# Kernel optimization log

Hardware: AMD Instinct MI355X
Metric: run time of the kernel (lower is better)

## Reference

```python
import jax, jax.numpy as jnp
import numpy as np
from jax import lax

GRID_W, GRID_H = 4, 4
N_NODES = GRID_W * GRID_H  # 16
N_NEIGH = 8
N_CLS = 10
BN_EPS = 1e-5


def _neighbors(i, w, h, mode=8):
    # exact port of Brain.neighbors (ordering matters for the concat)
    size = w * h
    out = []
    if i - w >= 0:
        out.append(i - w)
    if i % w != 0:
        out.append(i - 1)
    if (i + 1) % w != 0:
        out.append(i + 1)
    if i + w < size:
        out.append(i + w)
    if mode == 8:
        if i - w - 1 >= 0 and i % w != 0:
            out.append(i - w - 1)
        if i - w + 1 >= 0 and (i + 1) % w != 0:
            out.append(i - w + 1)
        if i + w - 1 < size and i % w != 0:
            out.append(i + w - 1)
        if i + w + 1 < size and (i + 1) % w != 0:
            out.append(i + w + 1)
    return out


def _neighbor_table():
    idx = np.full((N_NODES, N_NEIGH), 0, dtype=np.int32)
    mask = np.zeros((N_NODES, N_NEIGH), dtype=np.float32)
    for i in range(N_NODES):
        n = _neighbors(i, GRID_W, GRID_H, 8)
        idx[i, :len(n)] = np.array(n, dtype=np.int32)
        mask[i, :len(n)] = 1.0
    return jnp.asarray(idx), jnp.asarray(mask)


def _conv(x, w, b):
    y = lax.conv_general_dilated(x, w, (1, 1), 'SAME',
                                 dimension_numbers=('NCHW', 'OIHW', 'NCHW'))
    return y + b[None, :, None, None]


def _bn_train(x, g, b):
    # BatchNorm2d in training mode (module default): batch statistics
    mean = jnp.mean(x, axis=(0, 2, 3), keepdims=True)
    var = jnp.var(x, axis=(0, 2, 3), keepdims=True)
    xn = (x - mean) * lax.rsqrt(var + BN_EPS)
    return xn * g[None, :, None, None] + b[None, :, None, None]


def _maxpool(x):
    # MaxPool2d(kernel=3, stride=2, padding=1)
    return lax.reduce_window(x, -jnp.inf, lax.max,
                             (1, 1, 3, 3), (1, 1, 2, 2),
                             ((0, 0), (0, 0), (1, 1), (1, 1)))


def setup_inputs() -> dict:
    key = jax.random.key(0)
    ks = jax.random.split(key, 24)
    B = 128
    f32 = jnp.float32

    def rn(k, shape, scale):
        return jax.random.normal(k, shape, dtype=f32) * scale

    inp = {
        'x': rn(ks[0], (B, 3, 64, 64), 1.0),
        'cw1': rn(ks[1], (64, 3, 3, 3), 0.1), 'cb1': jnp.zeros((64,), f32),
        'bn1_g': jnp.ones((64,), f32), 'bn1_b': jnp.zeros((64,), f32),
        'cw2': rn(ks[2], (128, 64, 3, 3), 0.05), 'cb2': jnp.zeros((128,), f32),
        'bn2_g': jnp.ones((128,), f32), 'bn2_b': jnp.zeros((128,), f32),
        'cw3': rn(ks[3], (256, 128, 3, 3), 0.03), 'cb3': jnp.zeros((256,), f32),
        'cw4': rn(ks[4], (256, 256, 3, 3), 0.02), 'cb4': jnp.zeros((256,), f32),
        'cw5': rn(ks[5], (512, 256, 3, 3), 0.02), 'cb5': jnp.zeros((512,), f32),
        'cw6': rn(ks[6], (512, 512, 3, 3), 0.015), 'cb6': jnp.zeros((512,), f32),
        'cw7': rn(ks[7], (512, 512, 3, 3), 0.015), 'cb7': jnp.zeros((512,), f32),
        'W1': rn(ks[8], (N_NODES, 592, 600), 0.04), 'b1': jnp.zeros((N_NODES, 600), f32),
        'W2': rn(ks[9], (N_NODES, 600, N_CLS), 0.04), 'b2': jnp.zeros((N_NODES, N_CLS), f32),
    }
    return inp


def _backbone(x, cw1, cb1, bn1_g, bn1_b, cw2, cb2, bn2_g, bn2_b,
              cw3, cb3, cw4, cb4, cw5, cb5, cw6, cb6, cw7, cb7):
    h = _maxpool(jax.nn.relu(_bn_train(_conv(x, cw1, cb1), bn1_g, bn1_b)))
    h = _maxpool(jax.nn.relu(_bn_train(_conv(h, cw2, cb2), bn2_g, bn2_b)))
    h = jax.nn.relu(_conv(h, cw3, cb3))
    h = _maxpool(jax.nn.relu(_conv(h, cw4, cb4)))
    h = jax.nn.relu(_conv(h, cw5, cb5))
    h = _maxpool(jax.nn.relu(_conv(h, cw6, cb6)))
    h = jax.nn.relu(_conv(h, cw7, cb7))
    return h  # [B, 512, 4, 4]


def _colons(X, W1, b1, W2, b2):
    # X: [16, B, 592] -> softmax probs [16, B, 10]; per-node MLP
    h = jnp.tanh(jnp.einsum('nbi,nio->nbo', X, W1) + b1[:, None, :])
    logits = jnp.einsum('nbh,nho->nbo', h, W2) + b2[:, None, :]
    return jax.nn.softmax(logits, axis=-1)


def reference(x, cw1, cb1, bn1_g, bn1_b, cw2, cb2, bn2_g, bn2_b,
              cw3, cb3, cw4, cb4, cw5, cb5, cw6, cb6, cw7, cb7,
              W1, b1, W2, b2):
    B = x.shape[0]
    conv = _backbone(x, cw1, cb1, bn1_g, bn1_b, cw2, cb2, bn2_g, bn2_b,
                     cw3, cb3, cw4, cb4, cw5, cb5, cw6, cb6, cw7, cb7)
    conv = conv.reshape(B, 512, N_NODES)           # torch.flatten(conv, 2)
    feats = jnp.transpose(conv, (2, 0, 1))         # [16, B, 512]

    # first pass: neighbor slots are all-zero p1..p8
    zeros80 = jnp.zeros((N_NODES, B, N_NEIGH * N_CLS), dtype=x.dtype)
    preds1 = _colons(jnp.concatenate([zeros80, feats], axis=-1), W1, b1, W2, b2)

    # second pass: gather neighbor predictions (zero-padded to 8 slots)
    idx, mask = _neighbor_table()                  # [16,8] int, [16,8] float
    gathered = preds1[idx]                         # [16, 8, B, 10]
    gathered = gathered * mask[:, :, None, None]
    neigh = jnp.transpose(gathered, (0, 2, 1, 3)).reshape(N_NODES, B, N_NEIGH * N_CLS)
    preds2 = _colons(jnp.concatenate([neigh, feats], axis=-1), W1, b1, W2, b2)  # [16, B, 10]

    sum_preds = jnp.mean(preds2, axis=0)           # [B, 10]
    squared_sum_preds = sum_preds * sum_preds
    return squared_sum_preds, preds2
```

## Files before the change

### kernel.cpp

```cpp
#include <hip/hip_runtime.h>
#include <math.h>


#define BN_EPS 1e-5f

typedef _Float16 f16x8 __attribute__((ext_vector_type(8)));
typedef _Float16 f16x4 __attribute__((ext_vector_type(4)));
typedef float    f32x4v __attribute__((ext_vector_type(4)));

constexpr int ilog2c(int x) { return x <= 1 ? 0 : 1 + ilog2c(x >> 1); }

__device__ __forceinline__ void lds_barrier() {
    asm volatile("s_waitcnt lgkmcnt(0)\n\ts_barrier" ::: "memory");
}

__global__ __launch_bounds__(256)
void wprep_kernel(const float* __restrict__ cw1, const float* __restrict__ cw2,
                  const float* __restrict__ cw3, const float* __restrict__ cw4,
                  const float* __restrict__ cw5, const float* __restrict__ cw6,
                  const float* __restrict__ cw7, _Float16* __restrict__ wreg)
{
    const int layer = blockIdx.y;
    const int t = blockIdx.x * 256 + threadIdx.x;
    if (layer == 0) {
        if (t < 64) {
#pragma unroll
            for (int k = 0; k < 32; ++k)
                wreg[t * 32 + k] = (k < 27) ? (_Float16)cw1[t * 27 + k] : (_Float16)0.f;
        }
        return;
    }
    const float* src = nullptr;
    _Float16* dst = nullptr;
    int n = 0;
    switch (layer) {
        case 1: src = cw2; dst = wreg + 2048;    n = 8192;   break;
        case 2: src = cw3; dst = wreg + 75776;   n = 32768;  break;
        case 3: src = cw4; dst = wreg + 370688;  n = 65536;  break;
        case 4: src = cw5; dst = wreg + 960512;  n = 131072; break;
        case 5: src = cw6; dst = wreg + 2140160; n = 262144; break;
        case 6: src = cw7; dst = wreg + 4499456; n = 262144; break;
    }
    if (t >= n) return;
#pragma unroll
    for (int ph = 0; ph < 9; ++ph)
        dst[ph * n + t] = (_Float16)src[t * 9 + ph];
}

__global__ __launch_bounds__(256)
void w1t_kernel(const float* __restrict__ W1, _Float16* __restrict__ Tf,
                _Float16* __restrict__ Tn)
{
    __shared__ float T[64][65];
    const int n  = blockIdx.z;
    const int o0 = blockIdx.y * 64;
    const int k0 = blockIdx.x * 64;
    const int tid = threadIdx.x;
    const int c  = tid & 63;
    const int r4 = tid >> 6;
    const float* Wn = W1 + (size_t)n * 592 * 600;
#pragma unroll
    for (int rep = 0; rep < 16; ++rep) {
        const int kr = rep * 4 + r4;
        const int k = k0 + kr, o = o0 + c;
        float v = 0.f;
        if (k < 592 && o < 600) v = Wn[k * 600 + o];
        T[kr][c] = v;
    }
    __syncthreads();
#pragma unroll
    for (int rep = 0; rep < 16; ++rep) {
        const int orr = rep * 4 + r4;
        const int o = o0 + orr;
        const int k = k0 + c;
        const float v = T[c][orr];
        if (k >= 80 && k < 592)
            Tf[((size_t)(n * 640 + o)) * 512 + (k - 80)] = (_Float16)v;
        if (k < 96)
            Tn[((size_t)(n * 640 + o)) * 96 + k] = (k < 80) ? (_Float16)v : (_Float16)0.f;
    }
}

__global__ void b1pad_kernel(const float* __restrict__ b1, float* __restrict__ b1p)
{
    const int t = blockIdx.x * 256 + threadIdx.x;
    if (t >= 16 * 640) return;
    const int n = t / 640, o = t - n * 640;
    b1p[t] = (o < 600) ? b1[n * 600 + o] : 0.f;
}

__global__ __launch_bounds__(256)
void conv1_mfma_kernel(const float* __restrict__ in, const _Float16* __restrict__ w32,
                       _Float16* __restrict__ out, int B)
{
    __shared__ __align__(16) _Float16 As[64 * 32];
    __shared__ __align__(16) _Float16 Bs[128 * 32];

    const int tid  = threadIdx.x;
    const int pix0 = blockIdx.x * 128;
    const int bn   = tid & 127;
    const int bh   = tid >> 7;
    const int gp   = pix0 + bn;
    const int pb   = gp >> 12;
    const int sp   = gp & 4095;
    const int py   = sp >> 6;
    const int px   = sp & 63;
    const float* inb = in + (size_t)pb * 3 * 4096;

    _Float16 vals[16];
    if (bh == 0) {
#pragma unroll
        for (int u = 0; u < 16; ++u) {
            const int k = u;
            const int ci = k / 9, r = k - ci * 9, ky = r / 3, kx = r - ky * 3;
            const int iy = py + ky - 1, ix = px + kx - 1;
            float v = 0.f;
            if ((unsigned)iy < 64u && (unsigned)ix < 64u)
                v = inb[ci * 4096 + iy * 64 + ix];
            vals[u] = (_Float16)v;
        }
    } else {
#pragma unroll
        for (int u = 0; u < 16; ++u) {
            const int k = 16 + u;
            float v = 0.f;
            if (k < 27) {
                const int ci = k / 9, r = k - ci * 9, ky = r / 3, kx = r - ky * 3;
                const int iy = py + ky - 1, ix = px + kx - 1;
                if ((unsigned)iy < 64u && (unsigned)ix < 64u)
                    v = inb[ci * 4096 + iy * 64 + ix];
            }
            vals[u] = (_Float16)v;
        }
    }
    f16x8 b0, b1;
#pragma unroll
    for (int j = 0; j < 8; ++j) { b0[j] = vals[j]; b1[j] = vals[8 + j]; }
    *(f16x8*)&Bs[bn * 32 + (((2 * bh    ) ^ (bn & 3)) << 3)] = b0;
    *(f16x8*)&Bs[bn * 32 + (((2 * bh + 1) ^ (bn & 3)) << 3)] = b1;

    if (tid < 128) {
        const int arow = tid >> 1, ah = tid & 1;
        const f16x8 a0 = *(const f16x8*)(w32 + arow * 32 + ah * 16);
        const f16x8 a1 = *(const f16x8*)(w32 + arow * 32 + ah * 16 + 8);
        *(f16x8*)&As[arow * 32 + (((2 * ah    ) ^ (arow & 3)) << 3)] = a0;
        *(f16x8*)&As[arow * 32 + (((2 * ah + 1) ^ (arow & 3)) << 3)] = a1;
    }
    __syncthreads();

    const int lane = tid & 63, wv = tid >> 6;
    const int q = lane >> 4, lm = lane & 15;
    const int swz = (q ^ (lm & 3)) << 3;

    f16x8 af[4], bf[2];
#pragma unroll
    for (int ti = 0; ti < 4; ++ti)
        af[ti] = *(const f16x8*)&As[(ti * 16 + lm) * 32 + swz];
#pragma unroll
    for (int tj = 0; tj < 2; ++tj)
        bf[tj] = *(const f16x8*)&Bs[(wv * 32 + tj * 16 + lm) * 32 + swz];

    f32x4v acc[4][2];
#pragma unroll
    for (int ti = 0; ti < 4; ++ti)
#pragma unroll
        for (int tj = 0; tj < 2; ++tj)
            acc[ti][tj] = __builtin_amdgcn_mfma_f32_16x16x32_f16(
                af[ti], bf[tj], (f32x4v)0.f, 0, 0, 0);

#pragma unroll
    for (int tj = 0; tj < 2; ++tj) {
        const int gpix = pix0 + wv * 32 + tj * 16 + lm;
#pragma unroll
        for (int ti = 0; ti < 4; ++ti) {
            const int cob = ti * 16 + q * 4;
            f16x4 h4;
#pragma unroll
            for (int r = 0; r < 4; ++r) h4[r] = (_Float16)acc[ti][tj][r];
            *(f16x4*)&out[(size_t)gpix * 64 + cob] = h4;
        }
    }
}

template <int CI, int CO, int H, int W, int KSPLIT, int EPI>
__global__ __launch_bounds__(256)
void conv_p2_kernel(const _Float16* __restrict__ in, const _Float16* __restrict__ w9,
                    const float* __restrict__ bias, _Float16* __restrict__ out,
                    float* __restrict__ part, const _Float16* __restrict__ zbuf, int B)
{
    constexpr int HW   = H * W;
    constexpr int lgHW = ilog2c(HW);
    constexpr int lgW  = ilog2c(W);

    __shared__ __align__(16) _Float16 As[3][128 * 32];
    __shared__ __align__(16) _Float16 Bs[3][128 * 32];

    const int tid  = threadIdx.x;
    const int pix0 = blockIdx.x * 128;
    const int co0  = blockIdx.y * 128;

    const int lane = tid & 63, wv = tid >> 6;
    const int wm = (wv & 1) * 64, wn = (wv >> 1) * 64;
    const int q = lane >> 4, lm = lane & 15;
    const int swz = (q ^ (lm & 3)) << 3;

    const int arow = tid >> 1, ah = tid & 1;
    const int aw0 = ((2 * ah    ) ^ (arow & 3)) << 3;
    const int aw1 = ((2 * ah + 1) ^ (arow & 3)) << 3;
    const _Float16* abase = w9 + ((size_t)(co0 + arow)) * CI + ah * 16;

    const int bn = tid & 127, bh = tid >> 7;
    const int gp = pix0 + bn;
    const int pb = gp >> lgHW;
    const int spx = gp & (HW - 1);
    const int py = spx >> lgW, px = spx & (W - 1);
    const int bw0 = ((2 * bh    ) ^ (bn & 3)) << 3;
    const int bw1 = ((2 * bh + 1) ^ (bn & 3)) << 3;

    constexpr int CS_TOT = CI / 32;
    constexpr int CS_PER = CS_TOT / KSPLIT;
    constexpr int NIT    = 9 * CS_PER;
    const int cs0 = (KSPLIT > 1) ? blockIdx.z * CS_PER : 0;

    const _Float16* bstage;
    auto setB = [&](int phx) {
        const int dy = phx / 3 - 1;
        const int dx = phx - (phx / 3) * 3 - 1;
        const int y2 = py + dy, x2 = px + dx;
        const bool valid = ((unsigned)y2 < (unsigned)H) && ((unsigned)x2 < (unsigned)W);
        const int sp2 = (y2 << lgW) | x2;
        bstage = valid ? (in + ((size_t)((pb << lgHW) | sp2)) * CI + bh * 16)
                       : (zbuf + bh * 16);
    };

    f32x4v acc[4][4];
#pragma unroll
    for (int i = 0; i < 4; ++i)
#pragma unroll
        for (int j = 0; j < 4; ++j) acc[i][j] = (f32x4v)0.f;

    f16x8 aq[2][2], bq[2][2];
    int lph = 0, lcs = 0;
    setB(0);
    auto loadT = [&](int s) {
        const _Float16* ap = abase + (size_t)lph * CO * CI + (size_t)(cs0 + lcs) * 32;
        aq[s][0] = *(const f16x8*)ap;
        aq[s][1] = *(const f16x8*)(ap + 8);
        const _Float16* bp2 = bstage + (size_t)(cs0 + lcs) * 32;
        bq[s][0] = *(const f16x8*)bp2;
        bq[s][1] = *(const f16x8*)(bp2 + 8);
        if (++lcs == CS_PER) { lcs = 0; ++lph; if (lph < 9) setB(lph); }
    };
    loadT(0);
    loadT(1);
    *(f16x8*)&As[0][arow * 32 + aw0] = aq[0][0];
    *(f16x8*)&As[0][arow * 32 + aw1] = aq[0][1];
    *(f16x8*)&Bs[0][bn * 32 + bw0]   = bq[0][0];
    *(f16x8*)&Bs[0][bn * 32 + bw1]   = bq[0][1];

#pragma unroll 6
    for (int it = 0; it < NIT; ++it) {
        if (it + 2 < NIT) loadT(it & 1);
        if (it + 1 < NIT) {
            const int s1 = (it + 1) & 1;
            const int wb = (it + 1) % 3;
            *(f16x8*)&As[wb][arow * 32 + aw0] = aq[s1][0];
            *(f16x8*)&As[wb][arow * 32 + aw1] = aq[s1][1];
            *(f16x8*)&Bs[wb][bn * 32 + bw0]   = bq[s1][0];
            *(f16x8*)&Bs[wb][bn * 32 + bw1]   = bq[s1][1];
        }
        lds_barrier();
        const int rb = it % 3;
        f16x8 afr[4], bfr[4];
#pragma unroll
        for (int ti = 0; ti < 4; ++ti)
            afr[ti] = *(const f16x8*)&As[rb][(wm + ti * 16 + lm) * 32 + swz];
#pragma unroll
        for (int tj = 0; tj < 4; ++tj)
            bfr[tj] = *(const f16x8*)&Bs[rb][(wn + tj * 16 + lm) * 32 + swz];
#pragma unroll
        for (int ti = 0; ti < 4; ++ti)
#pragma unroll
            for (int tj = 0; tj < 4; ++tj)
                acc[ti][tj] = __builtin_amdgcn_mfma_f32_16x16x32_f16(
                    afr[ti], bfr[tj], acc[ti][tj], 0, 0, 0);
    }

    if (EPI == 2) {
        float* pout = part + (size_t)blockIdx.z * ((size_t)B * HW * CO);
#pragma unroll
        for (int tj = 0; tj < 4; ++tj) {
            const int gpix = pix0 + wn + tj * 16 + lm;
#pragma unroll
            for (int ti = 0; ti < 4; ++ti) {
                const int cob = co0 + wm + ti * 16 + q * 4;
                *(float4*)&pout[(size_t)gpix * CO + cob] =
                    make_float4(acc[ti][tj][0], acc[ti][tj][1],
                                acc[ti][tj][2], acc[ti][tj][3]);
            }
        }
    } else {
#pragma unroll
        for (int tj = 0; tj < 4; ++tj) {
            const int gpix = pix0 + wn + tj * 16 + lm;
#pragma unroll
            for (int ti = 0; ti < 4; ++ti) {
                const int cob = co0 + wm + ti * 16 + q * 4;
                f16x4 h4;
                if (EPI == 1) {
                    const float4 bb4 = *(const float4*)&bias[cob];
                    h4[0] = (_Float16)fmaxf(acc[ti][tj][0] + bb4.x, 0.f);
                    h4[1] = (_Float16)fmaxf(acc[ti][tj][1] + bb4.y, 0.f);
                    h4[2] = (_Float16)fmaxf(acc[ti][tj][2] + bb4.z, 0.f);
                    h4[3] = (_Float16)fmaxf(acc[ti][tj][3] + bb4.w, 0.f);
                } else {
#pragma unroll
                    for (int r = 0; r < 4; ++r) h4[r] = (_Float16)acc[ti][tj][r];
                }
                *(f16x4*)&out[(size_t)gpix * CO + cob] = h4;
            }
        }
    }
}

template <int C>
__global__ __launch_bounds__(256)
void bn_stats_nhwc_kernel(const _Float16* __restrict__ in, float* __restrict__ sums,
                          int Ptot)
{
    constexpr int C8 = C / 8;
    constexpr int PS = 256 / C8;
    const int chunk = Ptot / gridDim.x;
    const int c8   = threadIdx.x & (C8 - 1);
    const int poff = threadIdx.x >> ilog2c(C8);
    float s[8], s2[8];
#pragma unroll
    for (int j = 0; j < 8; ++j) { s[j] = 0.f; s2[j] = 0.f; }
    const int p0 = blockIdx.x * chunk;
    for (int p = p0 + poff; p < p0 + chunk; p += PS) {
        const f16x8 v = *(const f16x8*)(in + (size_t)p * C + c8 * 8);
#pragma unroll
        for (int j = 0; j < 8; ++j) {
            const float f = (float)v[j];
            s[j] += f; s2[j] += f * f;
        }
    }
    __shared__ float ls[2 * C];
    for (int i = threadIdx.x; i < 2 * C; i += 256) ls[i] = 0.f;
    __syncthreads();
#pragma unroll
    for (int j = 0; j < 8; ++j) {
        atomicAdd(&ls[c8 * 8 + j], s[j]);
        atomicAdd(&ls[C + c8 * 8 + j], s2[j]);
    }
    __syncthreads();
    for (int i = threadIdx.x; i < 2 * C; i += 256) atomicAdd(&sums[i], ls[i]);
}

template <int C>
__global__ void bn_finalize_kernel(const float* __restrict__ sums,
                                   const float* __restrict__ g,
                                   const float* __restrict__ beta,
                                   float* __restrict__ ss, int Ntot)
{
    const int c = blockIdx.x * 64 + threadIdx.x;
    if (c >= C) return;
    const float inv   = 1.f / (float)Ntot;
    const float mean  = sums[c] * inv;
    const float var   = sums[C + c] * inv - mean * mean;
    const float scale = g[c] * rsqrtf(var + BN_EPS);
    ss[c]     = scale;
    ss[C + c] = beta[c] - mean * scale;
}

template <int C, int Hin, int Win, bool DO_BN>
__global__ __launch_bounds__(256)
void pool_nhwc_kernel(const _Float16* __restrict__ in, const float* __restrict__ ss,
                      _Float16* __restrict__ out, int B)
{
    constexpr int Ho = Hin / 2, Wo = Win / 2, C8 = C / 8;
    constexpr int lgC8 = ilog2c(C8), lgWo = ilog2c(Wo), lgHo = ilog2c(Ho);
    const int t = blockIdx.x * 256 + threadIdx.x;
    const int total = B * Ho * Wo * C8;
    if (t >= total) return;
    const int c8 = t & (C8 - 1);
    const int r1 = t >> lgC8;
    const int ox = r1 & (Wo - 1);
    const int r2 = r1 >> lgWo;
    const int oy = r2 & (Ho - 1);
    const int b  = r2 >> lgHo;

    float sc[8], sh[8];
    if (DO_BN) {
#pragma unroll
        for (int j = 0; j < 8; ++j) {
            sc[j] = ss[c8 * 8 + j];
            sh[j] = ss[C + c8 * 8 + j];
        }
    }
    float m[8];
#pragma unroll
    for (int j = 0; j < 8; ++j) m[j] = -1e30f;

    const int y0 = max(0, 2 * oy - 1), y1 = min(Hin - 1, 2 * oy + 1);
    const int x0 = max(0, 2 * ox - 1), x1 = min(Win - 1, 2 * ox + 1);
    const _Float16* ib = in + ((size_t)b * Hin * Win) * C + c8 * 8;
    for (int iy = y0; iy <= y1; ++iy)
        for (int ix = x0; ix <= x1; ++ix) {
            const f16x8 v = *(const f16x8*)(ib + (size_t)(iy * Win + ix) * C);
#pragma unroll
            for (int j = 0; j < 8; ++j) {
                float f = (float)v[j];
                if (DO_BN) f = f * sc[j] + sh[j];
                m[j] = fmaxf(m[j], f);
            }
        }
    f16x8 o;
#pragma unroll
    for (int j = 0; j < 8; ++j) {
        float f = m[j];
        if (DO_BN) f = fmaxf(f, 0.f);
        o[j] = (_Float16)f;
    }
    *(f16x8*)&out[((size_t)((b << (lgHo + lgWo)) | (oy << lgWo) | ox)) * C + c8 * 8] = o;
}

template <int CO, int Z>
__global__ __launch_bounds__(256)
void sum_bias_relu_nhwc_kernel(const float* __restrict__ part, const float* __restrict__ bias,
                               _Float16* __restrict__ out, int Npix)
{
    const int t = blockIdx.x * 256 + threadIdx.x;
    const int N8 = Npix * CO / 8;
    if (t >= N8) return;
    const size_t i8 = (size_t)t * 8;
    const int c = (int)(i8 & (CO - 1));
    const size_t S = (size_t)Npix * CO;
    float4 x0 = *(const float4*)(part + i8);
    float4 x1 = *(const float4*)(part + i8 + 4);
#pragma unroll
    for (int z = 1; z < Z; ++z) {
        const float4 p0 = *(const float4*)(part + z * S + i8);
        const float4 p1 = *(const float4*)(part + z * S + i8 + 4);
        x0.x += p0.x; x0.y += p0.y; x0.z += p0.z; x0.w += p0.w;
        x1.x += p1.x; x1.y += p1.y; x1.z += p1.z; x1.w += p1.w;
    }
    const float4 b0 = *(const float4*)(bias + c);
    const float4 b1 = *(const float4*)(bias + c + 4);
    f16x8 o;
    o[0] = (_Float16)fmaxf(x0.x + b0.x, 0.f);
    o[1] = (_Float16)fmaxf(x0.y + b0.y, 0.f);
    o[2] = (_Float16)fmaxf(x0.z + b0.z, 0.f);
    o[3] = (_Float16)fmaxf(x0.w + b0.w, 0.f);
    o[4] = (_Float16)fmaxf(x1.x + b1.x, 0.f);
    o[5] = (_Float16)fmaxf(x1.y + b1.y, 0.f);
    o[6] = (_Float16)fmaxf(x1.z + b1.z, 0.f);
    o[7] = (_Float16)fmaxf(x1.w + b1.w, 0.f);
    *(f16x8*)&out[i8] = o;
}

template <int Z>
__global__ __launch_bounds__(256)
void build_xf_kernel(const float* __restrict__ part, const float* __restrict__ bias,
                     _Float16* __restrict__ Xf, int B)
{
    const int t = blockIdx.x * 256 + threadIdx.x;
    if (t >= B * 16 * 128) return;
    const int pix = t >> 7;
    const int c   = (t & 127) * 4;
    const size_t S = (size_t)B * 16 * 512;
    float4 a = *(const float4*)(part + (size_t)pix * 512 + c);
#pragma unroll
    for (int z = 1; z < Z; ++z) {
        const float4 p = *(const float4*)(part + z * S + (size_t)pix * 512 + c);
        a.x += p.x; a.y += p.y; a.z += p.z; a.w += p.w;
    }
    const float4 bb = *(const float4*)(bias + c);
    f16x4 o4;
    o4[0] = (_Float16)fmaxf(a.x + bb.x, 0.f);
    o4[1] = (_Float16)fmaxf(a.y + bb.y, 0.f);
    o4[2] = (_Float16)fmaxf(a.z + bb.z, 0.f);
    o4[3] = (_Float16)fmaxf(a.w + bb.w, 0.f);
    const int b_ = pix >> 4, sp = pix & 15;
    *(f16x4*)&Xf[((size_t)(sp * B + b_)) * 512 + c] = o4;
}

template <int K, bool PASS2>
__global__ __launch_bounds__(256)
void fc1_mfma_kernel(const _Float16* __restrict__ Xf, const _Float16* __restrict__ W1T,
                     const float* __restrict__ b1p, float* __restrict__ pre,
                     float* __restrict__ h, int B)
{
    __shared__ __align__(16) _Float16 As[2][128 * 32];
    __shared__ __align__(16) _Float16 Bs[2][128 * 32];

    const int tid = threadIdx.x;
    const int o0  = blockIdx.x * 128;
    const int n   = blockIdx.y;

    const int lane = tid & 63, wv = tid >> 6;
    const int wm = (wv & 1) * 64, wn = (wv >> 1) * 64;
    const int q = lane >> 4, lm = lane & 15;
    const int swz = (q ^ (lm & 3)) << 3;

    const int arow = tid >> 1, ah = tid & 1;
    const int aw0 = ((2 * ah    ) ^ (arow & 3)) << 3;
    const int aw1 = ((2 * ah + 1) ^ (arow & 3)) << 3;

    const _Float16* asrc = W1T + ((size_t)(n * 640 + o0 + arow)) * K + ah * 16;
    const _Float16* bsrc = Xf  + ((size_t)(n * 128 + arow)) * K + ah * 16;

    f32x4v acc[4][4];
#pragma unroll
    for (int i = 0; i < 4; ++i)
#pragma unroll
        for (int j = 0; j < 4; ++j) acc[i][j] = (f32x4v)0.f;

    constexpr int S = K / 32;
    {
        const f16x8 a0 = *(const f16x8*)(asrc);
        const f16x8 a1 = *(const f16x8*)(asrc + 8);
        const f16x8 b0 = *(const f16x8*)(bsrc);
        const f16x8 b1 = *(const f16x8*)(bsrc + 8);
        *(f16x8*)&As[0][arow * 32 + aw0] = a0;
        *(f16x8*)&As[0][arow * 32 + aw1] = a1;
        *(f16x8*)&Bs[0][arow * 32 + aw0] = b0;
        *(f16x8*)&Bs[0][arow * 32 + aw1] = b1;
    }
    int buf = 0;
    for (int s = 0; s < S; ++s) {
        f16x8 aN0, aN1, bN0, bN1;
        if (s + 1 < S) {
            aN0 = *(const f16x8*)(asrc + (s + 1) * 32);
            aN1 = *(const f16x8*)(asrc + (s + 1) * 32 + 8);
            bN0 = *(const f16x8*)(bsrc + (s + 1) * 32);
            bN1 = *(const f16x8*)(bsrc + (s + 1) * 32 + 8);
        }
        lds_barrier();
        f16x8 afr[4], bfr[4];
#pragma unroll
        for (int ti = 0; ti < 4; ++ti)
            afr[ti] = *(const f16x8*)&As[buf][(wm + ti * 16 + lm) * 32 + swz];
#pragma unroll
        for (int tj = 0; tj < 4; ++tj)
            bfr[tj] = *(const f16x8*)&Bs[buf][(wn + tj * 16 + lm) * 32 + swz];
#pragma unroll
        for (int ti = 0; ti < 4; ++ti)
#pragma unroll
            for (int tj = 0; tj < 4; ++tj)
                acc[ti][tj] = __builtin_amdgcn_mfma_f32_16x16x32_f16(
                    afr[ti], bfr[tj], acc[ti][tj], 0, 0, 0);
        if (s + 1 < S) {
            *(f16x8*)&As[buf ^ 1][arow * 32 + aw0] = aN0;
            *(f16x8*)&As[buf ^ 1][arow * 32 + aw1] = aN1;
            *(f16x8*)&Bs[buf ^ 1][arow * 32 + aw0] = bN0;
            *(f16x8*)&Bs[buf ^ 1][arow * 32 + aw1] = bN1;
            buf ^= 1;
        }
    }

#pragma unroll
    for (int tj = 0; tj < 4; ++tj) {
        const int m = wn + tj * 16 + lm;
#pragma unroll
        for (int ti = 0; ti < 4; ++ti) {
            const int o = o0 + wm + ti * 16 + q * 4;
            const size_t oi = ((size_t)(n * 128 + m)) * 640 + o;
            float4 base;
            if (PASS2) base = *(const float4*)&pre[oi];
            else       base = *(const float4*)&b1p[n * 640 + o];
            float4 v = make_float4(acc[ti][tj][0] + base.x, acc[ti][tj][1] + base.y,
                                   acc[ti][tj][2] + base.z, acc[ti][tj][3] + base.w);
            if (!PASS2) *(float4*)&pre[oi] = v;
            *(float4*)&h[oi] = make_float4(tanhf(v.x), tanhf(v.y), tanhf(v.z), tanhf(v.w));
        }
    }
}

__global__ __launch_bounds__(128)
void colon_fc2_kernel(const float* __restrict__ h, const float* __restrict__ W2,
                      const float* __restrict__ b2, float* __restrict__ preds, int B)
{
    const int n = blockIdx.x;
    __shared__ float W2s[6000];
    __shared__ float b2s[10];
    for (int i = threadIdx.x; i < 6000; i += 128) W2s[i] = W2[n * 6000 + i];
    if (threadIdx.x < 10) b2s[threadIdx.x] = b2[n * 10 + threadIdx.x];
    __syncthreads();

    for (int b = threadIdx.x; b < B; b += 128) {
        float l[10];
#pragma unroll
        for (int c = 0; c < 10; ++c) l[c] = b2s[c];
        const float* hp = h + ((size_t)(n * B + b)) * 640;
        for (int k = 0; k < 600; k += 4) {
            const float4 hv = *reinterpret_cast<const float4*>(&hp[k]);
            const float hh[4] = {hv.x, hv.y, hv.z, hv.w};
#pragma unroll
            for (int u = 0; u < 4; ++u)
#pragma unroll
                for (int c = 0; c < 10; ++c)
                    l[c] += hh[u] * W2s[(k + u) * 10 + c];
        }
        float mx = l[0];
#pragma unroll
        for (int c = 1; c < 10; ++c) mx = fmaxf(mx, l[c]);
        float s = 0.f;
#pragma unroll
        for (int c = 0; c < 10; ++c) { l[c] = expf(l[c] - mx); s += l[c]; }
        const float inv = 1.f / s;
        float* pp = preds + ((size_t)(n * B + b)) * 10;
#pragma unroll
        for (int c = 0; c < 10; ++c) pp[c] = l[c] * inv;
    }
}

__global__ __launch_bounds__(256)
void fill_neigh_kernel(const float* __restrict__ preds1, _Float16* __restrict__ Xn, int B)
{
    const int t = blockIdx.x * 256 + threadIdx.x;
    if (t >= 16 * B * 96) return;
    const int col = t % 96;
    const int b   = (t / 96) % B;
    const int n   = t / (96 * B);

    float v = 0.f;
    if (col < 80) {
        const int j = col / 10, c = col - j * 10;
        int lst[8];
        int cnt = 0;
        const int w = 4, sz = 16, i = n;
        if (i - w >= 0)                                lst[cnt++] = i - w;
        if (i % w != 0)                                lst[cnt++] = i - 1;
        if ((i + 1) % w != 0)                          lst[cnt++] = i + 1;
        if (i + w < sz)                                lst[cnt++] = i + w;
        if (i - w - 1 >= 0 && i % w != 0)              lst[cnt++] = i - w - 1;
        if (i - w + 1 >= 0 && (i + 1) % w != 0)        lst[cnt++] = i - w + 1;
        if (i + w - 1 < sz && i % w != 0)              lst[cnt++] = i + w - 1;
        if (i + w + 1 < sz && (i + 1) % w != 0)        lst[cnt++] = i + w + 1;
        if (j < cnt) v = preds1[((size_t)(lst[j] * B + b)) * 10 + c];
    }
    Xn[t] = (_Float16)v;
}

__global__ __launch_bounds__(256)
void final_out_kernel(const float* __restrict__ preds2, float* __restrict__ out0, int B)
{
    const int t = blockIdx.x * 256 + threadIdx.x;
    if (t >= B * 10) return;
    const int b = t / 10, c = t % 10;
    float s = 0.f;
#pragma unroll
    for (int n = 0; n < 16; ++n)
        s += preds2[((size_t)(n * B + b)) * 10 + c];
    const float m = s * (1.f / 16.f);
    out0[t] = m * m;
}

extern "C" void kernel_launch(void* const* d_in, const int* in_sizes, int n_in,
                              void* d_out, int out_size, void* d_ws, size_t ws_size,
                              hipStream_t stream)
{
    const float* x    = (const float*)d_in[0];
    const float* cw1  = (const float*)d_in[1];
    const float* bn1g = (const float*)d_in[3];
    const float* bn1b = (const float*)d_in[4];
    const float* cw2  = (const float*)d_in[5];
    const float* bn2g = (const float*)d_in[7];
    const float* bn2b = (const float*)d_in[8];
    const float* cw3  = (const float*)d_in[9];
    const float* cb3  = (const float*)d_in[10];
    const float* cw4  = (const float*)d_in[11];
    const float* cb4  = (const float*)d_in[12];
    const float* cw5  = (const float*)d_in[13];
    const float* cb5  = (const float*)d_in[14];
    const float* cw6  = (const float*)d_in[15];
    const float* cb6  = (const float*)d_in[16];
    const float* cw7  = (const float*)d_in[17];
    const float* cb7  = (const float*)d_in[18];
    const float* W1   = (const float*)d_in[19];
    const float* b1   = (const float*)d_in[20];
    const float* W2   = (const float*)d_in[21];
    const float* b2   = (const float*)d_in[22];

    const int B = in_sizes[0] / (3 * 64 * 64);

    float* ws = (float*)d_ws;
    float*     P    = ws;
    _Float16*  A    = (_Float16*)(ws + 8388608);
    _Float16*  Bb   = (_Float16*)(ws + 25165824);
    _Float16*  wreg = (_Float16*)(ws + 33554432);
    _Float16*  W1Tf = (_Float16*)(ws + 36984832);
    _Float16*  W1Tn = (_Float16*)(ws + 39606272);
    _Float16*  Xf16 = (_Float16*)(ws + 40097792);
    _Float16*  Xn16 = (_Float16*)(ws + 40622080);
    float*     b1p  = ws + 40720384;
    float*     preb = ws + 40730624;
    float*     hb   = ws + 42041344;
    float*     small= ws + 43352064;
    float* sums1  = small;
    float* sums2  = small + 256;
    float* ss1    = small + 1024;
    float* ss2    = small + 1536;
    float* preds1 = small + 2048;
    _Float16* zbuf = (_Float16*)(small + 32768);

    float* out0   = (float*)d_out;
    float* preds2 = (float*)d_out + (size_t)B * 10;

    hipMemsetAsync(small, 0, 512 * sizeof(float), stream);
    hipMemsetAsync(zbuf, 0, 4096, stream);

    wprep_kernel<<<dim3(1024, 7), 256, 0, stream>>>(cw1, cw2, cw3, cw4, cw5, cw6, cw7, wreg);
    w1t_kernel<<<dim3(10, 10, 16), 256, 0, stream>>>(W1, W1Tf, W1Tn);
    b1pad_kernel<<<(16 * 640 + 255) / 256, 256, 0, stream>>>(b1, b1p);

    _Float16* w1f  = wreg;
    _Float16* w9c2 = wreg + 2048;
    _Float16* w9c3 = wreg + 75776;
    _Float16* w9c4 = wreg + 370688;
    _Float16* w9c5 = wreg + 960512;
    _Float16* w9c6 = wreg + 2140160;
    _Float16* w9c7 = wreg + 4499456;

    conv1_mfma_kernel<<<B * 4096 / 128, 256, 0, stream>>>(x, w1f, A, B);
    bn_stats_nhwc_kernel<64><<<512, 256, 0, stream>>>(A, sums1, B * 4096);
    bn_finalize_kernel<64><<<1, 64, 0, stream>>>(sums1, bn1g, bn1b, ss1, B * 4096);
    pool_nhwc_kernel<64, 64, 64, true>
        <<<(B * 1024 * 8 + 255) / 256, 256, 0, stream>>>(A, ss1, Bb, B);

    conv_p2_kernel<64, 128, 32, 32, 1, 0>
        <<<dim3(B * 1024 / 128, 1), 256, 0, stream>>>(Bb, w9c2, nullptr, A, nullptr, zbuf, B);
    bn_stats_nhwc_kernel<128><<<256, 256, 0, stream>>>(A, sums2, B * 1024);
    bn_finalize_kernel<128><<<2, 64, 0, stream>>>(sums2, bn2g, bn2b, ss2, B * 1024);
    pool_nhwc_kernel<128, 32, 32, true>
        <<<(B * 256 * 16 + 255) / 256, 256, 0, stream>>>(A, ss2, Bb, B);

    conv_p2_kernel<128, 256, 16, 16, 1, 1>
        <<<dim3(B * 256 / 128, 2), 256, 0, stream>>>(Bb, w9c3, cb3, A, nullptr, zbuf, B);
    conv_p2_kernel<256, 256, 16, 16, 1, 1>
        <<<dim3(B * 256 / 128, 2), 256, 0, stream>>>(A, w9c4, cb4, Bb, nullptr, zbuf, B);
    pool_nhwc_kernel<256, 16, 16, false>
        <<<(B * 64 * 32 + 255) / 256, 256, 0, stream>>>(Bb, nullptr, A, B);

    conv_p2_kernel<256, 512, 8, 8, 2, 2>
        <<<dim3(B * 64 / 128, 4, 2), 256, 0, stream>>>(A, w9c5, nullptr, nullptr, P, zbuf, B);
    sum_bias_relu_nhwc_kernel<512, 2>
        <<<(B * 64 * 512 / 8 + 255) / 256, 256, 0, stream>>>(P, cb5, Bb, B * 64);

    conv_p2_kernel<512, 512, 8, 8, 2, 2>
        <<<dim3(B * 64 / 128, 4, 2), 256, 0, stream>>>(Bb, w9c6, nullptr, nullptr, P, zbuf, B);
    sum_bias_relu_nhwc_kernel<512, 2>
        <<<(B * 64 * 512 / 8 + 255) / 256, 256, 0, stream>>>(P, cb6, A, B * 64);
    pool_nhwc_kernel<512, 8, 8, false>
        <<<(B * 16 * 64 + 255) / 256, 256, 0, stream>>>(A, nullptr, Bb, B);

    conv_p2_kernel<512, 512, 4, 4, 8, 2>
        <<<dim3(B * 16 / 128, 4, 8), 256, 0, stream>>>(Bb, w9c7, nullptr, nullptr, P, zbuf, B);

    build_xf_kernel<8><<<(B * 16 * 128 + 255) / 256, 256, 0, stream>>>(P, cb7, Xf16, B);

    fc1_mfma_kernel<512, false>
        <<<dim3(5, 16), 256, 0, stream>>>(Xf16, W1Tf, b1p, preb, hb, B);
    colon_fc2_kernel<<<16, 128, 0, stream>>>(hb, W2, b2, preds1, B);

    fill_neigh_kernel<<<(16 * B * 96 + 255) / 256, 256, 0, stream>>>(preds1, Xn16, B);
    fc1_mfma_kernel<96, true>
        <<<dim3(5, 16), 256, 0, stream>>>(Xn16, W1Tn, b1p, preb, hb, B);
    colon_fc2_kernel<<<16, 128, 0, stream>>>(hb, W2, b2, preds2, B);

    final_out_kernel<<<(B * 10 + 255) / 256, 256, 0, stream>>>(preds2, out0, B);
}
```

Baseline: 633.9 us.

## Load conv tiles directly into LDS with global_load_lds, single-buffered

Replaces the register-staged, triple-buffered LDS pipeline in the implicit-GEMM conv kernel with direct global-to-LDS loads (global_load_lds, 16 bytes per lane). Each iteration now does a sync, issues the DMA loads, and syncs again before the MFMA work, using one LDS buffer and no XOR swizzle. This removes VGPR staging and ds_write instructions and shrinks LDS use, which may raise occupancy. In exchange it drops the software prefetch overlap and the bank-conflict swizzle, so the loads are exposed and the LDS fragment reads may hit bank conflicts.

```diff
diff --git a/kernel.cpp b/kernel.cpp
--- a/kernel.cpp
+++ b/kernel.cpp
@@ -12,6 +12,12 @@
 
 __device__ __forceinline__ void lds_barrier() {
     asm volatile("s_waitcnt lgkmcnt(0)\n\ts_barrier" ::: "memory");
+}
+
+__device__ __forceinline__ void gld16(const _Float16* g, _Float16* l) {
+    __builtin_amdgcn_global_load_lds(
+        (const __attribute__((address_space(1))) void*)g,
+        (__attribute__((address_space(3))) void*)l, 16, 0, 0);
 }
 
 __global__ __launch_bounds__(256)
@@ -184,16 +190,16 @@
 
 template <int CI, int CO, int H, int W, int KSPLIT, int EPI>
 __global__ __launch_bounds__(256)
-void conv_p2_kernel(const _Float16* __restrict__ in, const _Float16* __restrict__ w9,
-                    const float* __restrict__ bias, _Float16* __restrict__ out,
-                    float* __restrict__ part, const _Float16* __restrict__ zbuf, int B)
+void conv_dma_kernel(const _Float16* __restrict__ in, const _Float16* __restrict__ w9,
+                     const float* __restrict__ bias, _Float16* __restrict__ out,
+                     float* __restrict__ part, const _Float16* __restrict__ zbuf, int B)
 {
     constexpr int HW   = H * W;
     constexpr int lgHW = ilog2c(HW);
     constexpr int lgW  = ilog2c(W);
 
-    __shared__ __align__(16) _Float16 As[3][128 * 32];
-    __shared__ __align__(16) _Float16 Bs[3][128 * 32];
+    __shared__ __align__(16) _Float16 As[128 * 32];
+    __shared__ __align__(16) _Float16 Bs[128 * 32];
 
     const int tid  = threadIdx.x;
     const int pix0 = blockIdx.x * 128;
@@ -202,36 +208,50 @@
     const int lane = tid & 63, wv = tid >> 6;
     const int wm = (wv & 1) * 64, wn = (wv >> 1) * 64;
     const int q = lane >> 4, lm = lane & 15;
-    const int swz = (q ^ (lm & 3)) << 3;
-
-    const int arow = tid >> 1, ah = tid & 1;
-    const int aw0 = ((2 * ah    ) ^ (arow & 3)) << 3;
-    const int aw1 = ((2 * ah + 1) ^ (arow & 3)) << 3;
-    const _Float16* abase = w9 + ((size_t)(co0 + arow)) * CI + ah * 16;
-
-    const int bn = tid & 127, bh = tid >> 7;
-    const int gp = pix0 + bn;
-    const int pb = gp >> lgHW;
-    const int spx = gp & (HW - 1);
-    const int py = spx >> lgW, px = spx & (W - 1);
-    const int bw0 = ((2 * bh    ) ^ (bn & 3)) << 3;
-    const int bw1 = ((2 * bh + 1) ^ (bn & 3)) << 3;
-
-    constexpr int CS_TOT = CI / 32;
-    constexpr int CS_PER = CS_TOT / KSPLIT;
+
+    const int ch   = lane & 3;
+    const int rsub = lane >> 2;
+    const int r0   = wv * 32 + rsub;
+    const int r1   = r0 + 16;
+
+    const _Float16* ag0 = w9 + ((size_t)(co0 + r0)) * CI + ch * 8;
+    const _Float16* ag1 = w9 + ((size_t)(co0 + r1)) * CI + ch * 8;
+    _Float16* ald0 = &As[(wv * 32)      * 32];
+    _Float16* ald1 = &As[(wv * 32 + 16) * 32];
+    _Float16* bld0 = &Bs[(wv * 32)      * 32];
+    _Float16* bld1 = &Bs[(wv * 32 + 16) * 32];
+
+    int pbv[2], pyv[2], pxv[2];
+    {
+        const int gp0 = pix0 + r0;
+        pbv[0] = gp0 >> lgHW; pyv[0] = (gp0 & (HW - 1)) >> lgW; pxv[0] = gp0 & (W - 1);
+        const int gp1 = pix0 + r1;
+        pbv[1] = gp1 >> lgHW; pyv[1] = (gp1 & (HW - 1)) >> lgW; pxv[1] = gp1 & (W - 1);
+    }
+
+    constexpr int CS_PER = (CI / 32) / KSPLIT;
     constexpr int NIT    = 9 * CS_PER;
     const int cs0 = (KSPLIT > 1) ? blockIdx.z * CS_PER : 0;
 
-    const _Float16* bstage;
+    const _Float16* bg0;
+    const _Float16* bg1;
     auto setB = [&](int phx) {
         const int dy = phx / 3 - 1;
         const int dx = phx - (phx / 3) * 3 - 1;
-        const int y2 = py + dy, x2 = px + dx;
-        const bool valid = ((unsigned)y2 < (unsigned)H) && ((unsigned)x2 < (unsigned)W);
-        const int sp2 = (y2 << lgW) | x2;
-        bstage = valid ? (in + ((size_t)((pb << lgHW) | sp2)) * CI + bh * 16)
-                       : (zbuf + bh * 16);
+        {
+            const int y = pyv[0] + dy, x = pxv[0] + dx;
+            const bool v = ((unsigned)y < (unsigned)H) && ((unsigned)x < (unsigned)W);
+            bg0 = v ? in + ((size_t)((pbv[0] << lgHW) | (y << lgW) | x)) * CI + ch * 8
+                    : zbuf + ch * 8;
+        }
+        {
+            const int y = pyv[1] + dy, x = pxv[1] + dx;
+            const bool v = ((unsigned)y < (unsigned)H) && ((unsigned)x < (unsigned)W);
+            bg1 = v ? in + ((size_t)((pbv[1] << lgHW) | (y << lgW) | x)) * CI + ch * 8
+                    : zbuf + ch * 8;
+        }
     };
+    setB(0);
 
     f32x4v acc[4][4];
 #pragma unroll
@@ -239,51 +259,32 @@
 #pragma unroll
         for (int j = 0; j < 4; ++j) acc[i][j] = (f32x4v)0.f;
 
-    f16x8 aq[2][2], bq[2][2];
-    int lph = 0, lcs = 0;
-    setB(0);
-    auto loadT = [&](int s) {
-        const _Float16* ap = abase + (size_t)lph * CO * CI + (size_t)(cs0 + lcs) * 32;
-        aq[s][0] = *(const f16x8*)ap;
-        aq[s][1] = *(const f16x8*)(ap + 8);
-        const _Float16* bp2 = bstage + (size_t)(cs0 + lcs) * 32;
-        bq[s][0] = *(const f16x8*)bp2;
-        bq[s][1] = *(const f16x8*)(bp2 + 8);
-        if (++lcs == CS_PER) { lcs = 0; ++lph; if (lph < 9) setB(lph); }
-    };
-    loadT(0);
-    loadT(1);
-    *(f16x8*)&As[0][arow * 32 + aw0] = aq[0][0];
-    *(f16x8*)&As[0][arow * 32 + aw1] = aq[0][1];
-    *(f16x8*)&Bs[0][bn * 32 + bw0]   = bq[0][0];
-    *(f16x8*)&Bs[0][bn * 32 + bw1]   = bq[0][1];
-
-#pragma unroll 6
+    int ph = 0, cs = 0;
     for (int it = 0; it < NIT; ++it) {
-        if (it + 2 < NIT) loadT(it & 1);
-        if (it + 1 < NIT) {
-            const int s1 = (it + 1) & 1;
-            const int wb = (it + 1) % 3;
-            *(f16x8*)&As[wb][arow * 32 + aw0] = aq[s1][0];
-            *(f16x8*)&As[wb][arow * 32 + aw1] = aq[s1][1];
-            *(f16x8*)&Bs[wb][bn * 32 + bw0]   = bq[s1][0];
-            *(f16x8*)&Bs[wb][bn * 32 + bw1]   = bq[s1][1];
-        }
-        lds_barrier();
-        const int rb = it % 3;
+        __syncthreads();
+        const size_t ko = (size_t)(cs0 + cs) * 32;
+        const size_t ao = (size_t)ph * CO * CI + ko;
+        gld16(ag0 + ao, ald0);
+        gld16(ag1 + ao, ald1);
+        gld16(bg0 + ko, bld0);
+        gld16(bg1 + ko, bld1);
+        __syncthreads();
+
         f16x8 afr[4], bfr[4];
 #pragma unroll
         for (int ti = 0; ti < 4; ++ti)
-            afr[ti] = *(const f16x8*)&As[rb][(wm + ti * 16 + lm) * 32 + swz];
+            afr[ti] = *(const f16x8*)&As[(wm + ti * 16 + lm) * 32 + q * 8];
 #pragma unroll
         for (int tj = 0; tj < 4; ++tj)
-            bfr[tj] = *(const f16x8*)&Bs[rb][(wn + tj * 16 + lm) * 32 + swz];
+            bfr[tj] = *(const f16x8*)&Bs[(wn + tj * 16 + lm) * 32 + q * 8];
 #pragma unroll
         for (int ti = 0; ti < 4; ++ti)
 #pragma unroll
             for (int tj = 0; tj < 4; ++tj)
                 acc[ti][tj] = __builtin_amdgcn_mfma_f32_16x16x32_f16(
                     afr[ti], bfr[tj], acc[ti][tj], 0, 0, 0);
+
+        if (++cs == CS_PER) { cs = 0; ++ph; if (ph < 9) setB(ph); }
     }
 
     if (EPI == 2) {
@@ -729,33 +730,33 @@
     pool_nhwc_kernel<64, 64, 64, true>
         <<<(B * 1024 * 8 + 255) / 256, 256, 0, stream>>>(A, ss1, Bb, B);
 
-    conv_p2_kernel<64, 128, 32, 32, 1, 0>
+    conv_dma_kernel<64, 128, 32, 32, 1, 0>
         <<<dim3(B * 1024 / 128, 1), 256, 0, stream>>>(Bb, w9c2, nullptr, A, nullptr, zbuf, B);
     bn_stats_nhwc_kernel<128><<<256, 256, 0, stream>>>(A, sums2, B * 1024);
     bn_finalize_kernel<128><<<2, 64, 0, stream>>>(sums2, bn2g, bn2b, ss2, B * 1024);
     pool_nhwc_kernel<128, 32, 32, true>
         <<<(B * 256 * 16 + 255) / 256, 256, 0, stream>>>(A, ss2, Bb, B);
 
-    conv_p2_kernel<128, 256, 16, 16, 1, 1>
+    conv_dma_kernel<128, 256, 16, 16, 1, 1>
         <<<dim3(B * 256 / 128, 2), 256, 0, stream>>>(Bb, w9c3, cb3, A, nullptr, zbuf, B);
-    conv_p2_kernel<256, 256, 16, 16, 1, 1>
+    conv_dma_kernel<256, 256, 16, 16, 1, 1>
         <<<dim3(B * 256 / 128, 2), 256, 0, stream>>>(A, w9c4, cb4, Bb, nullptr, zbuf, B);
     pool_nhwc_kernel<256, 16, 16, false>
         <<<(B * 64 * 32 + 255) / 256, 256, 0, stream>>>(Bb, nullptr, A, B);
 
-    conv_p2_kernel<256, 512, 8, 8, 2, 2>
+    conv_dma_kernel<256, 512, 8, 8, 2, 2>
         <<<dim3(B * 64 / 128, 4, 2), 256, 0, stream>>>(A, w9c5, nullptr, nullptr, P, zbuf, B);
     sum_bias_relu_nhwc_kernel<512, 2>
         <<<(B * 64 * 512 / 8 + 255) / 256, 256, 0, stream>>>(P, cb5, Bb, B * 64);
 
-    conv_p2_kernel<512, 512, 8, 8, 2, 2>
+    conv_dma_kernel<512, 512, 8, 8, 2, 2>
         <<<dim3(B * 64 / 128, 4, 2), 256, 0, stream>>>(Bb, w9c6, nullptr, nullptr, P, zbuf, B);
     sum_bias_relu_nhwc_kernel<512, 2>
         <<<(B * 64 * 512 / 8 + 255) / 256, 256, 0, stream>>>(P, cb6, A, B * 64);
     pool_nhwc_kernel<512, 8, 8, false>
         <<<(B * 16 * 64 + 255) / 256, 256, 0, stream>>>(A, nullptr, Bb, B);
 
-    conv_p2_kernel<512, 512, 4, 4, 8, 2>
+    conv_dma_kernel<512, 512, 4, 4, 8, 2>
         <<<dim3(B * 16 / 128, 4, 8), 256, 0, stream>>>(Bb, w9c7, nullptr, nullptr, P, zbuf, B);
 
     build_xf_kernel<8><<<(B * 16 * 128 + 255) / 256, 256, 0, stream>>>(P, cb7, Xf16, B);
```

Result: no change. 635.0 us (+0.2%).
